# Performance work log

Measured on AMD Instinct MI355X. Metric: run time of the kernel, lower is better.

Reference implementation:

```python
import jax, jax.numpy as jnp
import numpy as np
from jax import lax

H, W = 4096, 4096

def setup_inputs() -> dict:
    key = jax.random.key(0)
    k_occ, k_seed = jax.random.split(key)
    occupied = (jax.random.uniform(k_occ, (H, W)) < 0.3).astype(jnp.float32)
    flood = ((jax.random.uniform(k_seed, (H, W)) < 1e-3).astype(jnp.float32)
             * (1.0 - occupied))
    flood_input = jnp.stack([occupied, flood], axis=-1)  # [H, W, 2]
    flood_count = jnp.zeros((H, W), dtype=jnp.float32)
    # Fixed flood kernel, HWIO layout: (3, 3, in=2, out=1)
    kernel = jnp.zeros((3, 3, 2, 1), dtype=jnp.float32)
    kernel = kernel.at[1, 1, 0, 0].set(-5.0)  # occupied center blocks flood
    kernel = kernel.at[1, 2, 1, 0].set(1.0)   # right
    kernel = kernel.at[2, 1, 1, 0].set(1.0)   # down
    kernel = kernel.at[1, 0, 1, 0].set(1.0)   # left
    kernel = kernel.at[0, 1, 1, 0].set(1.0)   # up
    kernel = kernel.at[1, 1, 1, 0].set(1.0)   # center
    bias = jnp.zeros((1,), dtype=jnp.float32)
    return {"flood_input": flood_input, "flood_count": flood_count,
            "kernel": kernel, "bias": bias, "num_steps": 16}

def reference(flood_input, flood_count, kernel, bias, num_steps):
    dn = ("NHWC", "HWIO", "NHWC")

    def flood_step(carry, _):
        x, count = carry                      # x: [H, W, 2], count: [H, W]
        occupied = x[..., 0]
        y = lax.conv_general_dilated(x[None], kernel, (1, 1), "SAME",
                                     dimension_numbers=dn)[0, ..., 0] + bias[0]
        y = jnp.clip(y, 0.0, 1.0)             # flooded frontier
        new_x = jnp.stack([occupied, y], axis=-1)
        return (new_x, count + y), None

    (x_final, count_final), _ = lax.scan(flood_step,
                                         (flood_input, flood_count),
                                         None, length=num_steps)
    # [H, W, 3]: occupied, flood, count
    return jnp.concatenate([x_final, count_final[..., None]], axis=-1)
```

## Files before the change

### kernel.cpp

```cpp
#include <hip/hip_runtime.h>


typedef unsigned long long u64;

#define HH 4096
#define WW 4096
#define WPR 64
#define TILE 96
#define HALO 16
#define REG 128
#define NSTEPS 16

__global__ __launch_bounds__(256) void pack_kernel(
    const float* __restrict__ flood_input,
    u64* __restrict__ occP, u64* __restrict__ flP)
{
    const int lane = threadIdx.x & 63;
    const int wv   = threadIdx.x >> 6;
    const int r    = blockIdx.x;
#pragma unroll
    for (int b = 0; b < 2; ++b) {
        float vx[8], vy[8];
#pragma unroll
        for (int j = 0; j < 8; ++j) {
            const int w = wv * 16 + b * 8 + j;
            const float2 v = *(const float2*)(flood_input +
                                ((size_t)r * WW + (w << 6) + lane) * 2);
            vx[j] = v.x; vy[j] = v.y;
        }
#pragma unroll
        for (int j = 0; j < 8; ++j) {
            const int w = wv * 16 + b * 8 + j;
            const u64 om = __ballot(vx[j] > 0.5f);
            const u64 fm = __ballot(vy[j] > 0.5f);
            if (lane == 0) {
                occP[(size_t)r * WPR + w] = om;
                flP [(size_t)r * WPR + w] = fm;
            }
        }
    }
}

__global__ __launch_bounds__(256, 8) void flood_kernel(
    const u64* __restrict__ occP, const u64* __restrict__ flP,
    const float* __restrict__ flood_count,
    float* __restrict__ out)
{
    __shared__ u64 occL[REG * 2];
    __shared__ u64 bufA[REG * 2];
    __shared__ u64 bufB[REG * 2];
    __shared__ u64 cntL[TILE * 2 * 5];

    const int tid  = threadIdx.x;
    const int lane = tid & 63;
    const int wv   = tid >> 6;

    const int tile_r0 = blockIdx.y * TILE;
    const int tile_c0 = blockIdx.x * TILE;
    const int row0 = tile_r0 - HALO;
    const int col0 = tile_c0 - HALO;

    const int r  = tid >> 1, h = tid & 1;
    const int gr = row0 + r;
    const bool rin = (gr >= 0) & (gr < HH);
    const int s  = col0 + (h << 6);
    const int q0 = ((s + 64) >> 6) - 1;
    const int sh = s - (q0 << 6);

    const size_t base = (size_t)(rin ? gr : 0) * WPR;
    const int qa = min(max(q0, 0), WPR - 1);
    const int qb = min(max(q0 + 1, 0), WPR - 1);
    u64 o0 = occP[base + qa], o1 = occP[base + qb];
    u64 f0 = flP [base + qa], f1 = flP [base + qb];
    const bool va = rin & (q0 >= 0);
    const bool vb = rin & (q0 + 1 < WPR);
    if (!va) { o0 = ~0ull; f0 = 0ull; }
    if (!vb) { o1 = ~0ull; f1 = 0ull; }
    const u64 occ = (o0 >> sh) | (sh ? (o1 << (64 - sh)) : 0ull);
    u64       f   = (f0 >> sh) | (sh ? (f1 << (64 - sh)) : 0ull);

    occL[tid] = occ;
    bufA[tid] = f;
    __syncthreads();

    u64 cnt0 = 0, cnt1 = 0, cnt2 = 0, cnt3 = 0, cnt4 = 0;
    const u64 nocc = ~occ;
    u64* cur = bufA;
    u64* nxt = bufB;
    for (int it = 0; it < NSTEPS; ++it) {
        const u64 up = (r > 0)       ? cur[tid - 2] : 0ull;
        const u64 dn = (r < REG - 1) ? cur[tid + 2] : 0ull;
        const u64 nb = cur[tid ^ 1];
        const u64 cl = h ? (nb >> 63) : 0ull;
        const u64 cr = h ? 0ull : (nb << 63);
        const u64 nf = nocc & (f | (f << 1) | cl | (f >> 1) | cr | up | dn);
        u64 c = nf, t;
        t = cnt0; cnt0 = t ^ c; c = t & c;
        t = cnt1; cnt1 = t ^ c; c = t & c;
        t = cnt2; cnt2 = t ^ c; c = t & c;
        t = cnt3; cnt3 = t ^ c; c = t & c;
        cnt4 ^= c;
        nxt[tid] = nf;
        f = nf;
        __syncthreads();
        u64* tmp = cur; cur = nxt; nxt = tmp;
    }

    if (r >= HALO && r < HALO + TILE) {
        const int rr = r - HALO;
        u64* c = &cntL[(rr * 2 + h) * 5];
        c[0] = cnt0; c[1] = cnt1; c[2] = cnt2; c[3] = cnt3; c[4] = cnt4;
    }
    __syncthreads();

#pragma unroll 2
    for (int orow = wv; orow < TILE; orow += 4) {
        const int grr = tile_r0 + orow;
        if (grr >= HH) continue;
        const int gc0 = tile_c0 + lane;
        const int gc1 = tile_c0 + 64 + lane;
        const bool v0 = gc0 < WW;
        const bool v1 = (lane < 32) && (gc1 < WW);
        const float fc0 = v0 ? flood_count[(size_t)grr * WW + gc0] : 0.f;
        const float fc1 = v1 ? flood_count[(size_t)grr * WW + gc1] : 0.f;
        const int rreg = orow + HALO;
#pragma unroll
        for (int sp = 0; sp < 2; ++sp) {
            const bool vv = sp ? v1 : v0;
            if (!vv) continue;
            const int oc  = (sp << 6) + lane;
            const int gc  = sp ? gc1 : gc0;
            const int creg = oc + HALO;
            const int word = creg >> 6, bit = creg & 63;
            const u64 ow = occL[rreg * 2 + word];
            const u64 fw = cur [rreg * 2 + word];
            const u64* cp = &cntL[(orow * 2 + word) * 5];
            int cv = 0;
#pragma unroll
            for (int k = 0; k < 5; ++k)
                cv += (int)((cp[k] >> bit) & 1ull) << k;
            float3 o3;
            o3.x = (float)((ow >> bit) & 1ull);
            o3.y = (float)((fw >> bit) & 1ull);
            o3.z = (float)cv + (sp ? fc1 : fc0);
            *(float3*)(out + ((size_t)grr * WW + gc) * 3) = o3;
        }
    }
}

extern "C" void kernel_launch(void* const* d_in, const int* in_sizes, int n_in,
                              void* d_out, int out_size, void* d_ws, size_t ws_size,
                              hipStream_t stream) {
    const float* flood_input = (const float*)d_in[0];
    const float* flood_cnt   = (const float*)d_in[1];
    float* out = (float*)d_out;

    u64* occP = (u64*)d_ws;
    u64* flP  = occP + (size_t)HH * WPR;

    pack_kernel<<<dim3(HH), dim3(256), 0, stream>>>(flood_input, occP, flP);

    dim3 grid((WW + TILE - 1) / TILE, (HH + TILE - 1) / TILE);
    flood_kernel<<<grid, dim3(256), 0, stream>>>(occP, flP, flood_cnt, out);
}
```

Baseline: 371.2 us.

## Use per-wavefront 64x64 bit tiles with shuffle-based neighbor exchange

Each wavefront now owns a 64-row by 64-bit window (32x32 output interior plus a 16-cell halo). Each lane holds one row word, and vertical neighbours come from wavefront shuffles instead of shared memory, which removes the per-step block barriers and LDS traffic. The cost is heavier halo redundancy: only 32 of 64 columns and 32 of 64 rows are kept, so bit-ops and packed loads per output cell roughly double. The output phase is also reorganised so half-wavefronts write 32-column rows.

Result: slower. 415.0 us (+11.8%).

```diff
diff --git a/kernel.cpp b/kernel.cpp
--- a/kernel.cpp
+++ b/kernel.cpp
@@ -6,10 +6,9 @@
 #define HH 4096
 #define WW 4096
 #define WPR 64
-#define TILE 96
+#define NSTEPS 16
 #define HALO 16
-#define REG 128
-#define NSTEPS 16
+#define IT 32
 
 __global__ __launch_bounds__(256) void pack_kernel(
     const float* __restrict__ flood_input,
@@ -46,26 +45,20 @@
     const float* __restrict__ flood_count,
     float* __restrict__ out)
 {
-    __shared__ u64 occL[REG * 2];
-    __shared__ u64 bufA[REG * 2];
-    __shared__ u64 bufB[REG * 2];
-    __shared__ u64 cntL[TILE * 2 * 5];
+    __shared__ u64 plane[4][IT][7];
 
     const int tid  = threadIdx.x;
     const int lane = tid & 63;
     const int wv   = tid >> 6;
 
-    const int tile_r0 = blockIdx.y * TILE;
-    const int tile_c0 = blockIdx.x * TILE;
-    const int row0 = tile_r0 - HALO;
-    const int col0 = tile_c0 - HALO;
+    const int tile_r0 = blockIdx.y * IT;
+    const int tile_c0 = blockIdx.x * (4 * IT) + wv * IT;
 
-    const int r  = tid >> 1, h = tid & 1;
-    const int gr = row0 + r;
+    const int gr  = tile_r0 - HALO + lane;
     const bool rin = (gr >= 0) & (gr < HH);
-    const int s  = col0 + (h << 6);
-    const int q0 = ((s + 64) >> 6) - 1;
-    const int sh = s - (q0 << 6);
+    const int s   = tile_c0 - HALO;
+    const int q0  = ((s + 64) >> 6) - 1;
+    const int sh  = s - (q0 << 6);
 
     const size_t base = (size_t)(rin ? gr : 0) * WPR;
     const int qa = min(max(q0, 0), WPR - 1);
@@ -79,72 +72,49 @@
     const u64 occ = (o0 >> sh) | (sh ? (o1 << (64 - sh)) : 0ull);
     u64       f   = (f0 >> sh) | (sh ? (f1 << (64 - sh)) : 0ull);
 
-    occL[tid] = occ;
-    bufA[tid] = f;
-    __syncthreads();
-
-    u64 cnt0 = 0, cnt1 = 0, cnt2 = 0, cnt3 = 0, cnt4 = 0;
     const u64 nocc = ~occ;
-    u64* cur = bufA;
-    u64* nxt = bufB;
+    u64 c0 = 0, c1 = 0, c2 = 0, c3 = 0, c4 = 0;
+#pragma unroll
     for (int it = 0; it < NSTEPS; ++it) {
-        const u64 up = (r > 0)       ? cur[tid - 2] : 0ull;
-        const u64 dn = (r < REG - 1) ? cur[tid + 2] : 0ull;
-        const u64 nb = cur[tid ^ 1];
-        const u64 cl = h ? (nb >> 63) : 0ull;
-        const u64 cr = h ? 0ull : (nb << 63);
-        const u64 nf = nocc & (f | (f << 1) | cl | (f >> 1) | cr | up | dn);
-        u64 c = nf, t;
-        t = cnt0; cnt0 = t ^ c; c = t & c;
-        t = cnt1; cnt1 = t ^ c; c = t & c;
-        t = cnt2; cnt2 = t ^ c; c = t & c;
-        t = cnt3; cnt3 = t ^ c; c = t & c;
-        cnt4 ^= c;
-        nxt[tid] = nf;
-        f = nf;
-        __syncthreads();
-        u64* tmp = cur; cur = nxt; nxt = tmp;
+        u64 up = __shfl_up(f, 1);
+        u64 dn = __shfl_down(f, 1);
+        if (lane == 0)  up = 0ull;
+        if (lane == 63) dn = 0ull;
+        f = nocc & (f | (f << 1) | (f >> 1) | up | dn);
+        u64 c = f, t;
+        t = c0; c0 = t ^ c; c = t & c;
+        t = c1; c1 = t ^ c; c = t & c;
+        t = c2; c2 = t ^ c; c = t & c;
+        t = c3; c3 = t ^ c; c = t & c;
+        c4 ^= c;
     }
 
-    if (r >= HALO && r < HALO + TILE) {
-        const int rr = r - HALO;
-        u64* c = &cntL[(rr * 2 + h) * 5];
-        c[0] = cnt0; c[1] = cnt1; c[2] = cnt2; c[3] = cnt3; c[4] = cnt4;
+    if (lane >= HALO && lane < HALO + IT) {
+        u64* p = plane[wv][lane - HALO];
+        p[0] = occ; p[1] = f;
+        p[2] = c0; p[3] = c1; p[4] = c2; p[5] = c3; p[6] = c4;
     }
     __syncthreads();
 
-#pragma unroll 2
-    for (int orow = wv; orow < TILE; orow += 4) {
-        const int grr = tile_r0 + orow;
-        if (grr >= HH) continue;
-        const int gc0 = tile_c0 + lane;
-        const int gc1 = tile_c0 + 64 + lane;
-        const bool v0 = gc0 < WW;
-        const bool v1 = (lane < 32) && (gc1 < WW);
-        const float fc0 = v0 ? flood_count[(size_t)grr * WW + gc0] : 0.f;
-        const float fc1 = v1 ? flood_count[(size_t)grr * WW + gc1] : 0.f;
-        const int rreg = orow + HALO;
+    const int half = lane >> 5;
+    const int col  = lane & 31;
+    const int gc   = tile_c0 + col;
+    const int bit  = HALO + col;
+#pragma unroll 4
+    for (int rp = 0; rp < IT; rp += 2) {
+        const int orow = rp + half;
+        const int grr  = tile_r0 + orow;
+        const float fc = flood_count[(size_t)grr * WW + gc];
+        const u64* p = plane[wv][orow];
+        int cv = 0;
 #pragma unroll
-        for (int sp = 0; sp < 2; ++sp) {
-            const bool vv = sp ? v1 : v0;
-            if (!vv) continue;
-            const int oc  = (sp << 6) + lane;
-            const int gc  = sp ? gc1 : gc0;
-            const int creg = oc + HALO;
-            const int word = creg >> 6, bit = creg & 63;
-            const u64 ow = occL[rreg * 2 + word];
-            const u64 fw = cur [rreg * 2 + word];
-            const u64* cp = &cntL[(orow * 2 + word) * 5];
-            int cv = 0;
-#pragma unroll
-            for (int k = 0; k < 5; ++k)
-                cv += (int)((cp[k] >> bit) & 1ull) << k;
-            float3 o3;
-            o3.x = (float)((ow >> bit) & 1ull);
-            o3.y = (float)((fw >> bit) & 1ull);
-            o3.z = (float)cv + (sp ? fc1 : fc0);
-            *(float3*)(out + ((size_t)grr * WW + gc) * 3) = o3;
-        }
+        for (int k = 0; k < 5; ++k)
+            cv += (int)((p[2 + k] >> bit) & 1ull) << k;
+        float3 o3;
+        o3.x = (float)((p[0] >> bit) & 1ull);
+        o3.y = (float)((p[1] >> bit) & 1ull);
+        o3.z = (float)cv + fc;
+        *(float3*)(out + ((size_t)grr * WW + gc) * 3) = o3;
     }
 }
 
@@ -160,6 +130,6 @@
 
     pack_kernel<<<dim3(HH), dim3(256), 0, stream>>>(flood_input, occP, flP);
 
-    dim3 grid((WW + TILE - 1) / TILE, (HH + TILE - 1) / TILE);
+    dim3 grid(WW / (4 * IT), HH / IT);
     flood_kernel<<<grid, dim3(256), 0, stream>>>(occP, flP, flood_cnt, out);
 }
```
